# Optimization experiments

Hardware: AMD Instinct MI355X
Metric: run time of the kernel (lower is better)

## Reference

```python
import jax, jax.numpy as jnp
import numpy as np

MAX_DISP = 48
PATCH = 3
OFFSET = 0
PAD = PATCH // 2
EPS = 1e-3


def _unfold(x, P, pad):
    # x: [B,C,H,W] -> [B,C,K2,H,W], K2 enumerated row-major over the PxP window
    B, C, H, W = x.shape
    xp = jnp.pad(x, ((0, 0), (0, 0), (pad, pad), (pad, pad)))
    return jnp.stack([xp[:, :, i:i + H, j:j + W]
                      for i in range(P) for j in range(P)], axis=2)


def _normalize(x, axes):
    # torch F.normalize: x / clamp(||x||_2, min=eps)
    n = jnp.sqrt(jnp.sum(x * x, axis=axes, keepdims=True))
    return x / jnp.maximum(n, EPS)


def setup_inputs() -> dict:
    key = jax.random.key(0)
    k1, k2, k3 = jax.random.split(key, 3)
    shp = (2, 32, 128, 416)
    return {
        "xl": jax.random.normal(k1, shp, dtype=jnp.float32),
        "xm": jax.random.normal(k2, shp, dtype=jnp.float32),
        "xr": jax.random.normal(k3, shp, dtype=jnp.float32),
    }


def reference(xl, xm, xr):
    B, C, H, W = xl.shape
    K2 = PATCH * PATCH
    scale = (C * K2) ** 0.5

    pl = _normalize(_unfold(xl, PATCH, PAD), (1, 2))  # [B,C,K2,H,W]
    pr = _normalize(_unfold(xr, PATCH, PAD), (1, 2))
    fl = _normalize(xm, (1,))                          # [B,C,H,W]

    # fl is constant over the K2 axis, so sum patches over K2 once for sim_L/sim_R
    Sl = pl.sum(axis=2)  # [B,C,H,W]
    Sr = pr.sum(axis=2)

    cL, cR, cLR = [], [], []
    for d in range(OFFSET, OFFSET + MAX_DISP):
        if d > 0:
            # shifted_l[w] = patches_l[w+d] (zero right pad); shifted_r[w] = patches_r[w-d]
            sL = jnp.einsum('bchw,bchw->bhw', fl[..., :W - d], Sl[..., d:])
            sL = jnp.pad(sL, ((0, 0), (0, 0), (0, d)))
            sR = jnp.einsum('bchw,bchw->bhw', fl[..., d:], Sr[..., :W - d])
            sR = jnp.pad(sR, ((0, 0), (0, 0), (d, 0)))
            wlr = W - 2 * d  # overlap region of the two opposite shifts
            if wlr > 0:
                sLR = jnp.einsum('bckhw,bckhw->bhw', pl[..., 2 * d:], pr[..., :wlr])
                sLR = jnp.pad(sLR, ((0, 0), (0, 0), (d, d)))
            else:
                sLR = jnp.zeros((B, H, W), xl.dtype)
        else:
            sL = jnp.einsum('bchw,bchw->bhw', fl, Sl)
            sR = jnp.einsum('bchw,bchw->bhw', fl, Sr)
            sLR = jnp.einsum('bckhw,bckhw->bhw', pl, pr)
        cL.append(sL / scale)
        cR.append(sR / scale)
        cLR.append(sLR / scale)

    cost = jnp.stack([jnp.stack(cL, 1), jnp.stack(cR, 1), jnp.stack(cLR, 1)], axis=1)
    return jnp.clip(cost, -10.0, 10.0).astype(jnp.float16)  # [B,3,D,H,W]
```

## Files before the change

kernel.cpp:

```cpp
#include <hip/hip_runtime.h>
#include <math.h>

#define B 2
#define C 32
#define H 128
#define W 416
#define D 48
#define HW (H*W)
#define CHW (C*HW)
#define EPSN 1e-3f
#define ISCALE 0.05892556509887896f
#define ESTR 36
#define LSTR 32
#define DSPL (D / 2)

__device__ __forceinline__ float clip10(float x) {
    return fminf(fmaxf(x, -10.0f), 10.0f);
}

#define FMA4(acc, f, k, u) acc += f[4*(k)+0]*(u).x + f[4*(k)+1]*(u).y \
                               + f[4*(k)+2]*(u).z + f[4*(k)+3]*(u).w;

#define CLW(v) ((v) < 0 ? 0 : ((v) > (W - 1) ? (W - 1) : (v)))

__global__ __launch_bounds__(256) void k_norm(const float* __restrict__ sql,
                                              const float* __restrict__ sqr,
                                              float* __restrict__ inl,
                                              float* __restrict__ inr) {
    int idx = blockIdx.x * 256 + threadIdx.x;
    if (idx >= B * HW) return;
    int b = idx / HW, hw = idx - b * HW;
    int h = hw / W, w = hw - h * W;
    float sl = 0.f, sr = 0.f;
#pragma unroll
    for (int di = -1; di <= 1; ++di) {
        int hh = h + di;
        if (hh < 0 || hh >= H) continue;
#pragma unroll
        for (int dj = -1; dj <= 1; ++dj) {
            int ww = w + dj;
            if (ww < 0 || ww >= W) continue;
            int p = b * HW + hh * W + ww;
            sl += sql[p];
            sr += sqr[p];
        }
    }
    inl[idx] = 1.0f / fmaxf(sqrtf(sl), EPSN);
    inr[idx] = 1.0f / fmaxf(sqrtf(sr), EPSN);
}

__device__ __forceinline__ void stage_row_v2(const float* __restrict__ gsrc,
                                             float* __restrict__ lds,
                                             int tid, int nthreads) {
    for (int t = tid; t < (W / 4) * C; t += nthreads) {
        int rw = t & 7;
        int cl = (t >> 3) & 7;
        int g  = t >> 6;
        int wg = g % 13;
        int ch = g / 13;
        int c  = ch * 8 + cl;
        int w4 = (wg * 8 + rw) * 4;
        float4 v = *(const float4*)(gsrc + (size_t)c * HW + w4);
        lds[(w4 + 0) * ESTR + c] = v.x;
        lds[(w4 + 1) * ESTR + c] = v.y;
        lds[(w4 + 2) * ESTR + c] = v.z;
        lds[(w4 + 3) * ESTR + c] = v.w;
    }
}

__device__ __forceinline__ void stage_row3_swz(const float* __restrict__ gsrc,
                                               float* __restrict__ lds,
                                               int h, int tid, int nthreads) {
    for (int t = tid; t < (W / 4) * C; t += nthreads) {
        int rw = t & 7;
        int cl = (t >> 3) & 7;
        int g  = t >> 6;
        int wg = g % 13;
        int ch = g / 13;
        int c  = ch * 8 + cl;
        int w4 = (wg * 8 + rw) * 4;
        const float* p = gsrc + (size_t)c * HW + w4;
        float4 v = *(const float4*)(p);
        if (h > 0) {
            float4 a = *(const float4*)(p - W);
            v.x += a.x; v.y += a.y; v.z += a.z; v.w += a.w;
        }
        if (h < H - 1) {
            float4 a = *(const float4*)(p + W);
            v.x += a.x; v.y += a.y; v.z += a.z; v.w += a.w;
        }
        int g2 = c >> 2, wd = c & 3;
        int k0 = (w4 >> 1) & 7;
        int k1 = (k0 + 1) & 7;
        lds[(w4 + 0) * LSTR + 4 * (g2 ^ k0) + wd] = v.x;
        lds[(w4 + 1) * LSTR + 4 * (g2 ^ k0) + wd] = v.y;
        lds[(w4 + 2) * LSTR + 4 * (g2 ^ k1) + wd] = v.z;
        lds[(w4 + 3) * LSTR + 4 * (g2 ^ k1) + wd] = v.w;
    }
}

__global__ __launch_bounds__(256) void k_lr(const float* __restrict__ xm,
                                            const float* __restrict__ xl,
                                            const float* __restrict__ xr,
                                            const float* __restrict__ inl,
                                            const float* __restrict__ inr,
                                            float* __restrict__ out) {
    __shared__ float sB[W * LSTR];
    __shared__ float sIn[W];
    int tid = threadIdx.x;
    int h = blockIdx.x;
    int b = blockIdx.y;
    int d0 = blockIdx.z * DSPL;
    bool act = tid < (W / 2);
    int w = 2 * tid;
    int bhw = b * HW + h * W;
    const float* pm = xm + (size_t)b * CHW + h * W;

    float fl0[C], fl1[C];
    if (act) {
        float am0 = 0.f, am1 = 0.f;
#pragma unroll
        for (int c = 0; c < C; ++c) {
            float2 mv = *(const float2*)(pm + (size_t)c * HW + w);
            fl0[c] = mv.x; fl1[c] = mv.y;
            am0 += mv.x * mv.x; am1 += mv.y * mv.y;
        }
        float im0 = 1.0f / fmaxf(sqrtf(am0), EPSN);
        float im1 = 1.0f / fmaxf(sqrtf(am1), EPSN);
#pragma unroll
        for (int c = 0; c < C; ++c) { fl0[c] *= im0; fl1[c] *= im1; }
    } else {
#pragma unroll
        for (int c = 0; c < C; ++c) { fl0[c] = 0.f; fl1[c] = 0.f; }
    }

    float4 RA0, RA1, RA2, RA3, RA4, RA5, RA6, RA7;
    float4 RB0, RB1, RB2, RB3, RB4, RB5, RB6, RB7;

#define LOADU(P, vv) { int _vq = CLW(vv); \
    const float4* _c4 = (const float4*)(sB + (size_t)_vq * LSTR); \
    int _ky = (_vq >> 1) & 7; \
    P##0 = _c4[_ky];     P##1 = _c4[1 ^ _ky]; P##2 = _c4[2 ^ _ky]; P##3 = _c4[3 ^ _ky]; \
    P##4 = _c4[4 ^ _ky]; P##5 = _c4[5 ^ _ky]; P##6 = _c4[6 ^ _ky]; P##7 = _c4[7 ^ _ky]; }

#define DOT2U(P, c0, c1) { float _x0=0.f,_x1=0.f,_y0=0.f,_y1=0.f; \
    FMA4(_x0, fl0, 0, P##0) FMA4(_x0, fl0, 1, P##1) FMA4(_x0, fl0, 2, P##2) FMA4(_x0, fl0, 3, P##3) \
    FMA4(_x1, fl0, 4, P##4) FMA4(_x1, fl0, 5, P##5) FMA4(_x1, fl0, 6, P##6) FMA4(_x1, fl0, 7, P##7) \
    FMA4(_y0, fl1, 0, P##0) FMA4(_y0, fl1, 1, P##1) FMA4(_y0, fl1, 2, P##2) FMA4(_y0, fl1, 3, P##3) \
    FMA4(_y1, fl1, 4, P##4) FMA4(_y1, fl1, 5, P##5) FMA4(_y1, fl1, 6, P##6) FMA4(_y1, fl1, 7, P##7) \
    c0 = _x0 + _x1; c1 = _y0 + _y1; }

    stage_row3_swz(xl + (size_t)b * CHW + h * W, sB, h, tid, 256);
    for (int j = tid; j < W; j += 256) sIn[j] = inl[bhw + j];
    __syncthreads();
    if (act) {
        float* oL = out + ((size_t)b * 3 + 0) * D * HW + h * W;
        const int vb = w + d0 - 1;
        float g0a = 0.f, g0b = 0.f, g1a = 0.f, g1b = 0.f, s0p = 0.f;
#define STEPL(P, jj) { int v = vb + (jj); bool ok = (v >= 0) && (v < W); \
    float c0, c1; DOT2U(P, c0, c1); c0 = ok ? c0 : 0.f; c1 = ok ? c1 : 0.f; \
    float s0 = 0.f, s1 = 0.f; \
    if ((jj) >= 2) { int m = v - 1; \
        if (m < W) { float sc = sIn[m] * ISCALE; \
            s0 = clip10((g0a + g0b + c0) * sc); s1 = clip10((g1a + g1b + c1) * sc); } \
        if ((jj) >= 3) { int d = d0 + (jj) - 3; \
            *(float2*)(oL + (size_t)d * HW + w) = make_float2(s0p, s1); } } \
    s0p = s0; g0a = g0b; g0b = c0; g1a = g1b; g1b = c1; }
        LOADU(RA, vb);
#pragma unroll 2
        for (int j = 0; j < DSPL + 2; j += 2) {
            LOADU(RB, vb + j + 1);
            STEPL(RA, j);
            LOADU(RA, vb + j + 2);
            STEPL(RB, j + 1);
        }
        STEPL(RA, DSPL + 2);
#undef STEPL
    }
    __syncthreads();

    stage_row3_swz(xr + (size_t)b * CHW + h * W, sB, h, tid, 256);
    for (int j = tid; j < W; j += 256) sIn[j] = inr[bhw + j];
    __syncthreads();
    if (act) {
        float* oR = out + ((size_t)b * 3 + 1) * D * HW + h * W;
        const int vb = w - d0 - DSPL;
        float g0a = 0.f, g0b = 0.f, g1a = 0.f, g1b = 0.f, s0p = 0.f;
#define STEPR(P, jj) { int v = vb + (jj); bool ok = (v >= 0) && (v < W); \
    float c0, c1; DOT2U(P, c0, c1); c0 = ok ? c0 : 0.f; c1 = ok ? c1 : 0.f; \
    float s0 = 0.f, s1 = 0.f; \
    if ((jj) >= 2) { int m = v - 1; \
        if (m >= 0) { float sc = sIn[m] * ISCALE; \
            s0 = clip10((g0a + g0b + c0) * sc); s1 = clip10((g1a + g1b + c1) * sc); } \
        if ((jj) >= 3) { int d = d0 + DSPL + 2 - (jj); \
            *(float2*)(oR + (size_t)d * HW + w) = make_float2(s0p, s1); } } \
    s0p = s0; g0a = g0b; g0b = c0; g1a = g1b; g1b = c1; }
        LOADU(RA, vb);
#pragma unroll 2
        for (int j = 0; j < DSPL + 2; j += 2) {
            LOADU(RB, vb + j + 1);
            STEPR(RA, j);
            LOADU(RA, vb + j + 2);
            STEPR(RB, j + 1);
        }
        STEPR(RA, DSPL + 2);
#undef STEPR
    }
#undef LOADU
#undef DOT2U
}

__global__ __launch_bounds__(448, 4) void k_e(const float* __restrict__ xl,
                                              const float* __restrict__ xr,
                                              float* __restrict__ EH,
                                              float* __restrict__ sql,
                                              float* __restrict__ sqr) {
    __shared__ float sXL[W * ESTR];
    int tid = threadIdx.x;
    int h = blockIdx.x;
    int b = blockIdx.y;
    int d0 = blockIdx.z * DSPL;
    int lane = tid & 63;
    int wv = tid >> 6;
    int v = wv * 62 + lane - 1;
    bool vin = (v >= 0) && (v < W);
    const float* br = xr + (size_t)b * CHW + h * W;

    float xrv[C];
#pragma unroll
    for (int c = 0; c < C; ++c) xrv[c] = vin ? br[c * HW + v] : 0.0f;

    stage_row_v2(xl + (size_t)b * CHW + h * W, sXL, tid, 448);
    __syncthreads();

    bool wr = (lane >= 1) && (lane <= 62) && (v < W);

    if (blockIdx.z == 0) {
        float sr_ = 0.f, sl_ = 0.f;
#pragma unroll
        for (int c = 0; c < C; ++c) sr_ += xrv[c] * xrv[c];
        if (vin) {
            const float4* c4 = (const float4*)(sXL + v * ESTR);
#pragma unroll
            for (int q = 0; q < 8; ++q) {
                float4 x = c4[q];
                sl_ += x.x * x.x + x.y * x.y + x.z * x.z + x.w * x.w;
            }
        }
        if (wr) {
            sqr[b * HW + h * W + v] = sr_;
            sql[b * HW + h * W + v] = sl_;
        }
    }

    float* pe = EH + (((size_t)b * D) * H + h) * W + v;

    float4 RA0, RA1, RA2, RA3, RA4, RA5, RA6, RA7;
    float4 RB0, RB1, RB2, RB3, RB4, RB5, RB6, RB7;

#define LOADE(P, col) { int _vq = CLW(col); \
    const float4* _c4 = (const float4*)(sXL + (size_t)_vq * ESTR); \
    P##0 = _c4[0]; P##1 = _c4[1]; P##2 = _c4[2]; P##3 = _c4[3]; \
    P##4 = _c4[4]; P##5 = _c4[5]; P##6 = _c4[6]; P##7 = _c4[7]; }
#define STEPE(P, dd) { float _a = 0.f, _b = 0.f; \
    FMA4(_a, xrv, 0, P##0) FMA4(_a, xrv, 1, P##1) FMA4(_a, xrv, 2, P##2) FMA4(_a, xrv, 3, P##3) \
    FMA4(_b, xrv, 4, P##4) FMA4(_b, xrv, 5, P##5) FMA4(_b, xrv, 6, P##6) FMA4(_b, xrv, 7, P##7) \
    float e = (vin && (v + 2 * (dd)) < W) ? (_a + _b) : 0.f; \
    float em = __shfl_up(e, 1); \
    float ep = __shfl_down(e, 1); \
    float eh = em + e + ep; \
    if (wr) pe[(size_t)(dd) * HW] = eh; }

    LOADE(RA, v + 2 * d0);
#pragma unroll 2
    for (int d = d0; d < d0 + DSPL; d += 2) {
        LOADE(RB, v + 2 * d + 2);
        STEPE(RA, d);
        LOADE(RA, v + 2 * d + 4);
        STEPE(RB, d + 1);
    }
#undef LOADE
#undef STEPE
}

#define DCH 12
__global__ __launch_bounds__(448) void k_lr2(const float* __restrict__ EH,
                                             const float* __restrict__ inl,
                                             const float* __restrict__ inr,
                                             float* __restrict__ out) {
    int w = threadIdx.x;
    int dc = blockIdx.x;
    int h = blockIdx.y;
    int b = blockIdx.z;
    if (w >= W) return;
    int bhw = b * HW + h * W;
    bool hm = (h > 0), hp = (h < H - 1);

    float* o = out + ((size_t)b * 3 + 2) * D * HW + h * W + w;
#pragma unroll
    for (int i = 0; i < DCH; ++i) {
        int d = dc * DCH + i;
        float r = 0.0f;
        if (w >= d && w + d < W) {
            int vc = w - d;
            const float* base = EH + ((size_t)b * D + d) * HW + vc;
            float e = base[h * W];
            if (hm) e += base[(h - 1) * W];
            if (hp) e += base[(h + 1) * W];
            float nl = inl[bhw + w + d];
            float nr = inr[bhw + vc];
            r = clip10(e * nl * nr * ISCALE);
        }
        o[(size_t)d * HW] = r;
    }
}

extern "C" void kernel_launch(void* const* d_in, const int* in_sizes, int n_in,
                              void* d_out, int out_size, void* d_ws, size_t ws_size,
                              hipStream_t stream) {
    const float* xl = (const float*)d_in[0];
    const float* xm = (const float*)d_in[1];
    const float* xr = (const float*)d_in[2];
    float* out = (float*)d_out;

    float* ws = (float*)d_ws;
    float* inl = ws;
    float* inr = inl + B * HW;
    float* sql = inr + B * HW;
    float* sqr = sql + B * HW;
    float* EH  = sqr + B * HW;

    k_e<<<dim3(H, B, 2), dim3(448), 0, stream>>>(xl, xr, EH, sql, sqr);
    k_norm<<<dim3((B * HW + 255) / 256), dim3(256), 0, stream>>>(sql, sqr, inl, inr);
    k_lr<<<dim3(H, B, 2), dim3(256), 0, stream>>>(xm, xl, xr, inl, inr, out);
    k_lr2<<<dim3(4, H, B), dim3(448), 0, stream>>>(EH, inl, inr, out);
}
```

Baseline: 164.7 us.

## Use fp16 packed dot products in k_lr and store EH intermediate as fp16

k_lr now holds the normalized xm features as packed half pairs and stages the 3-row summed left/right features into LDS as fp16 pairs, with a new swizzle. The dot products use the fdot2 builtin instead of scalar fp32 FMAs, which halves LDS footprint and read traffic and cuts ALU work. The intermediate EH buffer written by k_e and read by k_lr2 becomes fp16, halving that global memory traffic. The cost is reduced precision in the inputs to the dot products and in the stored intermediate, although the final output is fp16 and clipped anyway.

```diff
diff --git a/kernel.cpp b/kernel.cpp
--- a/kernel.cpp
+++ b/kernel.cpp
@@ -11,11 +11,24 @@
 #define EPSN 1e-3f
 #define ISCALE 0.05892556509887896f
 #define ESTR 36
-#define LSTR 32
 #define DSPL (D / 2)
+
+typedef _Float16 h16;
+typedef _Float16 __attribute__((ext_vector_type(2))) h16x2;
 
 __device__ __forceinline__ float clip10(float x) {
     return fminf(fmaxf(x, -10.0f), 10.0f);
+}
+
+__device__ __forceinline__ float fdot2(h16x2 a, h16x2 bb, float c) {
+    return __builtin_amdgcn_fdot2(a, bb, c, false);
+}
+__device__ __forceinline__ h16x2 u2h(unsigned int u) {
+    union { unsigned int u; h16x2 h; } cv; cv.u = u; return cv.h;
+}
+__device__ __forceinline__ unsigned int pkh(float a, float bb) {
+    union { h16x2 h; unsigned int u; } cv;
+    cv.h = h16x2{(h16)a, (h16)bb}; return cv.u;
 }
 
 #define FMA4(acc, f, k, u) acc += f[4*(k)+0]*(u).x + f[4*(k)+1]*(u).y \
@@ -68,35 +81,54 @@
     }
 }
 
-__device__ __forceinline__ void stage_row3_swz(const float* __restrict__ gsrc,
-                                               float* __restrict__ lds,
-                                               int h, int tid, int nthreads) {
-    for (int t = tid; t < (W / 4) * C; t += nthreads) {
-        int rw = t & 7;
-        int cl = (t >> 3) & 7;
-        int g  = t >> 6;
-        int wg = g % 13;
-        int ch = g / 13;
-        int c  = ch * 8 + cl;
-        int w4 = (wg * 8 + rw) * 4;
-        const float* p = gsrc + (size_t)c * HW + w4;
-        float4 v = *(const float4*)(p);
+__device__ __forceinline__ void stage_row3_h(const float* __restrict__ gsrc,
+                                             unsigned int* __restrict__ lds,
+                                             int h, int tid, int nthreads) {
+    for (int t = tid; t < (W / 4) * (C / 2); t += nthreads) {
+        int p = t & 15;
+        int u = t >> 4;
+        int v0 = 4 * u;
+        const float* pa = gsrc + (size_t)(2 * p) * HW + v0;
+        const float* pb = pa + HW;
+        float4 va = *(const float4*)pa;
+        float4 vb = *(const float4*)pb;
         if (h > 0) {
-            float4 a = *(const float4*)(p - W);
-            v.x += a.x; v.y += a.y; v.z += a.z; v.w += a.w;
+            float4 xa = *(const float4*)(pa - W);
+            float4 xb = *(const float4*)(pb - W);
+            va.x += xa.x; va.y += xa.y; va.z += xa.z; va.w += xa.w;
+            vb.x += xb.x; vb.y += xb.y; vb.z += xb.z; vb.w += xb.w;
         }
         if (h < H - 1) {
-            float4 a = *(const float4*)(p + W);
-            v.x += a.x; v.y += a.y; v.z += a.z; v.w += a.w;
-        }
-        int g2 = c >> 2, wd = c & 3;
-        int k0 = (w4 >> 1) & 7;
-        int k1 = (k0 + 1) & 7;
-        lds[(w4 + 0) * LSTR + 4 * (g2 ^ k0) + wd] = v.x;
-        lds[(w4 + 1) * LSTR + 4 * (g2 ^ k0) + wd] = v.y;
-        lds[(w4 + 2) * LSTR + 4 * (g2 ^ k1) + wd] = v.z;
-        lds[(w4 + 3) * LSTR + 4 * (g2 ^ k1) + wd] = v.w;
-    }
+            float4 xa = *(const float4*)(pa + W);
+            float4 xb = *(const float4*)(pb + W);
+            va.x += xa.x; va.y += xa.y; va.z += xa.z; va.w += xa.w;
+            vb.x += xb.x; vb.y += xb.y; vb.z += xb.z; vb.w += xb.w;
+        }
+        int q = p >> 2, lo = p & 3;
+        unsigned int pk0 = pkh(va.x, vb.x);
+        unsigned int pk1 = pkh(va.y, vb.y);
+        unsigned int pk2 = pkh(va.z, vb.z);
+        unsigned int pk3 = pkh(va.w, vb.w);
+#define PUTH(vv, val) { int _v = (vv); \
+    lds[16 * (_v ^ ((_v >> 1) & 1)) \
+        + 4 * (q ^ ((((_v) >> 1) ^ ((_v) >> 2)) & 3)) + lo] = (val); }
+        PUTH(v0 + 0, pk0)
+        PUTH(v0 + 1, pk1)
+        PUTH(v0 + 2, pk2)
+        PUTH(v0 + 3, pk3)
+#undef PUTH
+    }
+}
+
+__device__ __forceinline__ float dot32e(const float* __restrict__ x,
+                                        const float* __restrict__ col) {
+    const float4* c4 = (const float4*)col;
+    float4 u0 = c4[0], u1 = c4[1], u2 = c4[2], u3 = c4[3];
+    float4 u4 = c4[4], u5 = c4[5], u6 = c4[6], u7 = c4[7];
+    float a = 0.f, bb = 0.f;
+    FMA4(a, x, 0, u0) FMA4(a, x, 1, u1) FMA4(a, x, 2, u2) FMA4(a, x, 3, u3)
+    FMA4(bb, x, 4, u4) FMA4(bb, x, 5, u5) FMA4(bb, x, 6, u6) FMA4(bb, x, 7, u7)
+    return a + bb;
 }
 
 __global__ __launch_bounds__(256) void k_lr(const float* __restrict__ xm,
@@ -105,7 +137,7 @@
                                             const float* __restrict__ inl,
                                             const float* __restrict__ inr,
                                             float* __restrict__ out) {
-    __shared__ float sB[W * LSTR];
+    __shared__ unsigned int sBu[W * 16];
     __shared__ float sIn[W];
     int tid = threadIdx.x;
     int h = blockIdx.x;
@@ -116,41 +148,58 @@
     int bhw = b * HW + h * W;
     const float* pm = xm + (size_t)b * CHW + h * W;
 
-    float fl0[C], fl1[C];
+    h16x2 f0h[16], f1h[16];
     if (act) {
+        float t0[C], t1[C];
         float am0 = 0.f, am1 = 0.f;
 #pragma unroll
         for (int c = 0; c < C; ++c) {
             float2 mv = *(const float2*)(pm + (size_t)c * HW + w);
-            fl0[c] = mv.x; fl1[c] = mv.y;
+            t0[c] = mv.x; t1[c] = mv.y;
             am0 += mv.x * mv.x; am1 += mv.y * mv.y;
         }
         float im0 = 1.0f / fmaxf(sqrtf(am0), EPSN);
         float im1 = 1.0f / fmaxf(sqrtf(am1), EPSN);
 #pragma unroll
-        for (int c = 0; c < C; ++c) { fl0[c] *= im0; fl1[c] *= im1; }
+        for (int j = 0; j < 16; ++j) {
+            f0h[j] = h16x2{(h16)(t0[2 * j] * im0), (h16)(t0[2 * j + 1] * im0)};
+            f1h[j] = h16x2{(h16)(t1[2 * j] * im1), (h16)(t1[2 * j + 1] * im1)};
+        }
     } else {
 #pragma unroll
-        for (int c = 0; c < C; ++c) { fl0[c] = 0.f; fl1[c] = 0.f; }
-    }
-
-    float4 RA0, RA1, RA2, RA3, RA4, RA5, RA6, RA7;
-    float4 RB0, RB1, RB2, RB3, RB4, RB5, RB6, RB7;
-
-#define LOADU(P, vv) { int _vq = CLW(vv); \
-    const float4* _c4 = (const float4*)(sB + (size_t)_vq * LSTR); \
-    int _ky = (_vq >> 1) & 7; \
-    P##0 = _c4[_ky];     P##1 = _c4[1 ^ _ky]; P##2 = _c4[2 ^ _ky]; P##3 = _c4[3 ^ _ky]; \
-    P##4 = _c4[4 ^ _ky]; P##5 = _c4[5 ^ _ky]; P##6 = _c4[6 ^ _ky]; P##7 = _c4[7 ^ _ky]; }
-
-#define DOT2U(P, c0, c1) { float _x0=0.f,_x1=0.f,_y0=0.f,_y1=0.f; \
-    FMA4(_x0, fl0, 0, P##0) FMA4(_x0, fl0, 1, P##1) FMA4(_x0, fl0, 2, P##2) FMA4(_x0, fl0, 3, P##3) \
-    FMA4(_x1, fl0, 4, P##4) FMA4(_x1, fl0, 5, P##5) FMA4(_x1, fl0, 6, P##6) FMA4(_x1, fl0, 7, P##7) \
-    FMA4(_y0, fl1, 0, P##0) FMA4(_y0, fl1, 1, P##1) FMA4(_y0, fl1, 2, P##2) FMA4(_y0, fl1, 3, P##3) \
-    FMA4(_y1, fl1, 4, P##4) FMA4(_y1, fl1, 5, P##5) FMA4(_y1, fl1, 6, P##6) FMA4(_y1, fl1, 7, P##7) \
-    c0 = _x0 + _x1; c1 = _y0 + _y1; }
-
-    stage_row3_swz(xl + (size_t)b * CHW + h * W, sB, h, tid, 256);
+        for (int j = 0; j < 16; ++j) { f0h[j] = h16x2{(h16)0.f, (h16)0.f};
+                                       f1h[j] = h16x2{(h16)0.f, (h16)0.f}; }
+    }
+
+    uint4 RA0, RA1, RA2, RA3;
+    uint4 RB0, RB1, RB2, RB3;
+
+#define LOADH(P, vv) { int _v = CLW(vv); \
+    const uint4* _c4 = (const uint4*)(sBu + 16 * (_v ^ ((_v >> 1) & 1))); \
+    int _ky = ((_v >> 1) ^ (_v >> 2)) & 3; \
+    P##0 = _c4[_ky]; P##1 = _c4[1 ^ _ky]; P##2 = _c4[2 ^ _ky]; P##3 = _c4[3 ^ _ky]; }
+
+#define DOTH(P, c0, c1) { \
+    float _a0 = 0.f, _a1 = 0.f, _b0 = 0.f, _b1 = 0.f; \
+    _a0 = fdot2(f0h[0],  u2h((P##0).x), _a0); _a0 = fdot2(f0h[1],  u2h((P##0).y), _a0); \
+    _a0 = fdot2(f0h[2],  u2h((P##0).z), _a0); _a0 = fdot2(f0h[3],  u2h((P##0).w), _a0); \
+    _a0 = fdot2(f0h[4],  u2h((P##1).x), _a0); _a0 = fdot2(f0h[5],  u2h((P##1).y), _a0); \
+    _a0 = fdot2(f0h[6],  u2h((P##1).z), _a0); _a0 = fdot2(f0h[7],  u2h((P##1).w), _a0); \
+    _a1 = fdot2(f0h[8],  u2h((P##2).x), _a1); _a1 = fdot2(f0h[9],  u2h((P##2).y), _a1); \
+    _a1 = fdot2(f0h[10], u2h((P##2).z), _a1); _a1 = fdot2(f0h[11], u2h((P##2).w), _a1); \
+    _a1 = fdot2(f0h[12], u2h((P##3).x), _a1); _a1 = fdot2(f0h[13], u2h((P##3).y), _a1); \
+    _a1 = fdot2(f0h[14], u2h((P##3).z), _a1); _a1 = fdot2(f0h[15], u2h((P##3).w), _a1); \
+    _b0 = fdot2(f1h[0],  u2h((P##0).x), _b0); _b0 = fdot2(f1h[1],  u2h((P##0).y), _b0); \
+    _b0 = fdot2(f1h[2],  u2h((P##0).z), _b0); _b0 = fdot2(f1h[3],  u2h((P##0).w), _b0); \
+    _b0 = fdot2(f1h[4],  u2h((P##1).x), _b0); _b0 = fdot2(f1h[5],  u2h((P##1).y), _b0); \
+    _b0 = fdot2(f1h[6],  u2h((P##1).z), _b0); _b0 = fdot2(f1h[7],  u2h((P##1).w), _b0); \
+    _b1 = fdot2(f1h[8],  u2h((P##2).x), _b1); _b1 = fdot2(f1h[9],  u2h((P##2).y), _b1); \
+    _b1 = fdot2(f1h[10], u2h((P##2).z), _b1); _b1 = fdot2(f1h[11], u2h((P##2).w), _b1); \
+    _b1 = fdot2(f1h[12], u2h((P##3).x), _b1); _b1 = fdot2(f1h[13], u2h((P##3).y), _b1); \
+    _b1 = fdot2(f1h[14], u2h((P##3).z), _b1); _b1 = fdot2(f1h[15], u2h((P##3).w), _b1); \
+    c0 = _a0 + _a1; c1 = _b0 + _b1; }
+
+    stage_row3_h(xl + (size_t)b * CHW + h * W, sBu, h, tid, 256);
     for (int j = tid; j < W; j += 256) sIn[j] = inl[bhw + j];
     __syncthreads();
     if (act) {
@@ -158,7 +207,7 @@
         const int vb = w + d0 - 1;
         float g0a = 0.f, g0b = 0.f, g1a = 0.f, g1b = 0.f, s0p = 0.f;
 #define STEPL(P, jj) { int v = vb + (jj); bool ok = (v >= 0) && (v < W); \
-    float c0, c1; DOT2U(P, c0, c1); c0 = ok ? c0 : 0.f; c1 = ok ? c1 : 0.f; \
+    float c0, c1; DOTH(P, c0, c1); c0 = ok ? c0 : 0.f; c1 = ok ? c1 : 0.f; \
     float s0 = 0.f, s1 = 0.f; \
     if ((jj) >= 2) { int m = v - 1; \
         if (m < W) { float sc = sIn[m] * ISCALE; \
@@ -166,12 +215,12 @@
         if ((jj) >= 3) { int d = d0 + (jj) - 3; \
             *(float2*)(oL + (size_t)d * HW + w) = make_float2(s0p, s1); } } \
     s0p = s0; g0a = g0b; g0b = c0; g1a = g1b; g1b = c1; }
-        LOADU(RA, vb);
+        LOADH(RA, vb);
 #pragma unroll 2
         for (int j = 0; j < DSPL + 2; j += 2) {
-            LOADU(RB, vb + j + 1);
+            LOADH(RB, vb + j + 1);
             STEPL(RA, j);
-            LOADU(RA, vb + j + 2);
+            LOADH(RA, vb + j + 2);
             STEPL(RB, j + 1);
         }
         STEPL(RA, DSPL + 2);
@@ -179,7 +228,7 @@
     }
     __syncthreads();
 
-    stage_row3_swz(xr + (size_t)b * CHW + h * W, sB, h, tid, 256);
+    stage_row3_h(xr + (size_t)b * CHW + h * W, sBu, h, tid, 256);
     for (int j = tid; j < W; j += 256) sIn[j] = inr[bhw + j];
     __syncthreads();
     if (act) {
@@ -187,7 +236,7 @@
         const int vb = w - d0 - DSPL;
         float g0a = 0.f, g0b = 0.f, g1a = 0.f, g1b = 0.f, s0p = 0.f;
 #define STEPR(P, jj) { int v = vb + (jj); bool ok = (v >= 0) && (v < W); \
-    float c0, c1; DOT2U(P, c0, c1); c0 = ok ? c0 : 0.f; c1 = ok ? c1 : 0.f; \
+    float c0, c1; DOTH(P, c0, c1); c0 = ok ? c0 : 0.f; c1 = ok ? c1 : 0.f; \
     float s0 = 0.f, s1 = 0.f; \
     if ((jj) >= 2) { int m = v - 1; \
         if (m >= 0) { float sc = sIn[m] * ISCALE; \
@@ -195,24 +244,24 @@
         if ((jj) >= 3) { int d = d0 + DSPL + 2 - (jj); \
             *(float2*)(oR + (size_t)d * HW + w) = make_float2(s0p, s1); } } \
     s0p = s0; g0a = g0b; g0b = c0; g1a = g1b; g1b = c1; }
-        LOADU(RA, vb);
+        LOADH(RA, vb);
 #pragma unroll 2
         for (int j = 0; j < DSPL + 2; j += 2) {
-            LOADU(RB, vb + j + 1);
+            LOADH(RB, vb + j + 1);
             STEPR(RA, j);
-            LOADU(RA, vb + j + 2);
+            LOADH(RA, vb + j + 2);
             STEPR(RB, j + 1);
         }
         STEPR(RA, DSPL + 2);
 #undef STEPR
     }
-#undef LOADU
-#undef DOT2U
+#undef LOADH
+#undef DOTH
 }
 
 __global__ __launch_bounds__(448, 4) void k_e(const float* __restrict__ xl,
                                               const float* __restrict__ xr,
-                                              float* __restrict__ EH,
+                                              _Float16* __restrict__ EH,
                                               float* __restrict__ sql,
                                               float* __restrict__ sqr) {
     __shared__ float sXL[W * ESTR];
@@ -253,7 +302,7 @@
         }
     }
 
-    float* pe = EH + (((size_t)b * D) * H + h) * W + v;
+    _Float16* pe = EH + (((size_t)b * D) * H + h) * W + v;
 
     float4 RA0, RA1, RA2, RA3, RA4, RA5, RA6, RA7;
     float4 RB0, RB1, RB2, RB3, RB4, RB5, RB6, RB7;
@@ -269,7 +318,7 @@
     float em = __shfl_up(e, 1); \
     float ep = __shfl_down(e, 1); \
     float eh = em + e + ep; \
-    if (wr) pe[(size_t)(dd) * HW] = eh; }
+    if (wr) pe[(size_t)(dd) * HW] = (_Float16)eh; }
 
     LOADE(RA, v + 2 * d0);
 #pragma unroll 2
@@ -284,7 +333,7 @@
 }
 
 #define DCH 12
-__global__ __launch_bounds__(448) void k_lr2(const float* __restrict__ EH,
+__global__ __launch_bounds__(448) void k_lr2(const _Float16* __restrict__ EH,
                                              const float* __restrict__ inl,
                                              const float* __restrict__ inr,
                                              float* __restrict__ out) {
@@ -303,10 +352,10 @@
         float r = 0.0f;
         if (w >= d && w + d < W) {
             int vc = w - d;
-            const float* base = EH + ((size_t)b * D + d) * HW + vc;
-            float e = base[h * W];
-            if (hm) e += base[(h - 1) * W];
-            if (hp) e += base[(h + 1) * W];
+            const _Float16* base = EH + ((size_t)b * D + d) * HW + vc;
+            float e = (float)base[h * W];
+            if (hm) e += (float)base[(h - 1) * W];
+            if (hp) e += (float)base[(h + 1) * W];
             float nl = inl[bhw + w + d];
             float nr = inr[bhw + vc];
             r = clip10(e * nl * nr * ISCALE);
@@ -328,7 +377,7 @@
     float* inr = inl + B * HW;
     float* sql = inr + B * HW;
     float* sqr = sql + B * HW;
-    float* EH  = sqr + B * HW;
+    _Float16* EH = (_Float16*)(sqr + B * HW);
 
     k_e<<<dim3(H, B, 2), dim3(448), 0, stream>>>(xl, xr, EH, sql, sqr);
     k_norm<<<dim3((B * HW + 255) / 256), dim3(256), 0, stream>>>(sql, sqr, inl, inr);
```

Result: no change. 164.3 us (-0.2%).
